# Kernel optimization log

Hardware: AMD Instinct MI355X
Metric: run time of the kernel (lower is better)

Reference implementation:

```python
import jax, jax.numpy as jnp
import numpy as np

B = 8192
IN = 1024
H = 1024


def setup_inputs() -> dict:
    key = jax.random.key(0)
    ks = jax.random.split(key, 7)
    stdv = 1.0 / np.sqrt(H)
    u = lambda k, shape: jax.random.uniform(k, shape, jnp.float32, -stdv, stdv)
    return {
        "input": jax.random.normal(ks[0], (B, IN), jnp.float32),
        "h_prev": jax.random.normal(ks[1], (B, H), jnp.float32),
        "c_prev": jax.random.normal(ks[2], (B, H), jnp.float32),
        "W_ih": u(ks[3], (4 * H, IN)),
        "b_ih": u(ks[4], (4 * H,)),
        "W_hh": u(ks[5], (4 * H, H)),
        "b_hh": u(ks[6], (4 * H,)),
    }


def reference(input, h_prev, c_prev, W_ih, b_ih, W_hh, b_hh):
    # gates: [B, 4H] = input @ W_ih^T + b_ih + h_prev @ W_hh^T + b_hh
    gates = (jnp.einsum("bi,gi->bg", input, W_ih) + b_ih
             + jnp.einsum("bh,gh->bg", h_prev, W_hh) + b_hh)
    i_in, f_in, g_in, o_in = jnp.split(gates, 4, axis=1)
    i_t = jax.nn.sigmoid(i_in)
    f_t = jax.nn.sigmoid(f_in)
    g_t = jnp.tanh(g_in)
    o_t = jax.nn.sigmoid(o_in)
    c_t = f_t * c_prev + i_t * g_t
    h_t = o_t * jnp.tanh(c_t)
    return (h_t, c_t)
```

## Files before the change

### kernel.cpp

```cpp
#include <hip/hip_runtime.h>
#include <hip/hip_bf16.h>
#include <stdint.h>


typedef __attribute__((ext_vector_type(8))) __bf16 bf16x8;
typedef __attribute__((ext_vector_type(8))) unsigned short u16x8;
typedef __attribute__((ext_vector_type(4))) float f32x4;

__device__ __forceinline__ unsigned short f2bf(float f) {
  union { float f; unsigned int u; } v; v.f = f;
  unsigned int r = v.u + 0x7FFFu + ((v.u >> 16) & 1u);
  return (unsigned short)(r >> 16);
}

__global__ void cvt_all(const float* __restrict__ s0, const float* __restrict__ s1,
                        const float* __restrict__ s2, const float* __restrict__ s3,
                        unsigned short* __restrict__ d0, unsigned short* __restrict__ d1,
                        unsigned short* __restrict__ d2, unsigned short* __restrict__ d3) {
  const float* src; unsigned short* dst; int n8;
  if (blockIdx.y == 0)      { src = s0; dst = d0; n8 = 8192 * 128; }
  else if (blockIdx.y == 1) { src = s1; dst = d1; n8 = 8192 * 128; }
  else if (blockIdx.y == 2) { src = s2; dst = d2; n8 = 4096 * 128; }
  else                      { src = s3; dst = d3; n8 = 4096 * 128; }
  int i = blockIdx.x * blockDim.x + threadIdx.x;
  int stride = gridDim.x * blockDim.x;
  for (; i < n8; i += stride) {
    float4 a = ((const float4*)src)[2 * i];
    float4 b = ((const float4*)src)[2 * i + 1];
    u16x8 o;
    o[0] = f2bf(a.x); o[1] = f2bf(a.y); o[2] = f2bf(a.z); o[3] = f2bf(a.w);
    o[4] = f2bf(b.x); o[5] = f2bf(b.y); o[6] = f2bf(b.z); o[7] = f2bf(b.w);
    *(u16x8*)&dst[(size_t)i * 8] = o;
  }
}

#define STAGE_HALF(G) do {                                                     \
    const int t_ = (G) >> 2, j_ = (G) & 3;                                     \
    const int hks_ = j_ >> 1, isB_ = j_ & 1;                                   \
    const unsigned short* bA_; const unsigned short* bB_; int kk_;             \
    if (t_ < 16) { bA_ = Xb; bB_ = Wihb; kk_ = t_ * 64; }                      \
    else         { bA_ = Hb; bB_ = Whhb; kk_ = (t_ - 16) * 64; }               \
    const int col_ = kk_ + hks_ * 32 + scol;                                   \
    char* lb_ = smem + (((G) & 7) * 16384);                                    \
    _Pragma("unroll")                                                          \
    for (int r_ = 0; r_ < 2; ++r_) {                                           \
      const int row_ = r_ * 128 + srow;                                        \
      const unsigned short* src_ = isB_                                        \
          ? bB_ + (size_t)((row_ >> 6) * 1024 + h0 + (row_ & 63)) * 1024 + col_\
          : bA_ + (size_t)(m0 + row_) * 1024 + col_;                           \
      __builtin_amdgcn_global_load_lds(                                        \
          (const __attribute__((address_space(1))) void*)src_,                 \
          (__attribute__((address_space(3))) void*)(lb_ + r_ * 8192 + tid * 16),\
          16, 0, 0);                                                           \
    }                                                                          \
  } while (0)

#define PHASE(T, B, P) do {                                                    \
    const int ks_ = (P) >> 1, mh_ = (P) & 1;                                   \
    const char* sa_ = smem + (4 * (B) + 2 * ks_) * 16384;                      \
    const char* sb_ = smem + (4 * (B) + 2 * ks_ + 1) * 16384;                  \
    bf16x8 af_[4], bf_[4];                                                     \
    _Pragma("unroll")                                                          \
    for (int m2 = 0; m2 < 4; ++m2) {                                           \
      u16x8 t8 = *(const u16x8*)(sa_ +                                         \
          ((wr * 128 + (mh_ * 4 + m2) * 16 + l15) * 64 + l4 * 16));            \
      af_[m2] = __builtin_bit_cast(bf16x8, t8);                                \
    }                                                                          \
    _Pragma("unroll")                                                          \
    for (int n_ = 0; n_ < 4; ++n_) {                                           \
      u16x8 t8 = *(const u16x8*)(sb_ +                                         \
          ((wc * 64 + n_ * 16 + l15) * 64 + l4 * 16));                         \
      bf_[n_] = __builtin_bit_cast(bf16x8, t8);                                \
    }                                                                          \
    if (4 * (T) + 6 + (P) < 128) { STAGE_HALF(4 * (T) + 6 + (P)); }            \
    __builtin_amdgcn_s_barrier();                                              \
    __builtin_amdgcn_s_setprio(1);                                             \
    _Pragma("unroll")                                                          \
    for (int m2 = 0; m2 < 4; ++m2)                                             \
      _Pragma("unroll")                                                        \
      for (int n_ = 0; n_ < 4; ++n_)                                           \
        acc[mh_ * 4 + m2][n_] = __builtin_amdgcn_mfma_f32_16x16x32_bf16(       \
            af_[m2], bf_[n_], acc[mh_ * 4 + m2][n_], 0, 0, 0);                 \
    __builtin_amdgcn_s_setprio(0);                                             \
    __builtin_amdgcn_s_barrier();                                              \
  } while (0)

#define TILE(T, B) do {                                                        \
    PHASE(T, B, 0); PHASE(T, B, 1); PHASE(T, B, 2); PHASE(T, B, 3);            \
    if ((T) < 31) {                                                            \
      if ((T) == 30) { asm volatile("s_waitcnt vmcnt(0)" ::: "memory"); }      \
      else           { asm volatile("s_waitcnt vmcnt(4)" ::: "memory"); }      \
      __builtin_amdgcn_s_barrier();                                            \
    }                                                                          \
  } while (0)

__global__ __launch_bounds__(512, 2) void lstm_fused(
    const unsigned short* __restrict__ Xb, const unsigned short* __restrict__ Hb,
    const unsigned short* __restrict__ Wihb, const unsigned short* __restrict__ Whhb,
    const float* __restrict__ bih, const float* __restrict__ bhh,
    const float* __restrict__ cprev, float* __restrict__ out) {
  __shared__ __align__(16) char smem[131072];

  const int tid = threadIdx.x;
  const int lane = tid & 63;
  const int wid = tid >> 6;
  const int wr = wid >> 2;
  const int wc = wid & 3;
  const int l15 = lane & 15;
  const int l4 = lane >> 4;

  const int bid = blockIdx.x;
  const int tile_id = (bid & 7) * 64 + (bid >> 3);
  const int m0 = (tile_id >> 4) * 256;
  const int h0 = (tile_id & 15) * 64;

  const int srow = tid >> 2;
  const int scol = (tid & 3) * 8;

  f32x4 acc[8][4];
#pragma unroll
  for (int m = 0; m < 8; ++m)
#pragma unroll
    for (int n = 0; n < 4; ++n) {
      f32x4 z = {0.f, 0.f, 0.f, 0.f};
      acc[m][n] = z;
    }

  STAGE_HALF(0); STAGE_HALF(1); STAGE_HALF(2);
  STAGE_HALF(3); STAGE_HALF(4); STAGE_HALF(5);
  asm volatile("s_waitcnt vmcnt(4)" ::: "memory");
  __builtin_amdgcn_s_barrier();

#pragma unroll 1
  for (int th = 0; th < 16; ++th) {
    const int t0 = th * 2;
    TILE(t0, 0);
    TILE(t0 + 1, 1);
  }

  __syncthreads();
#pragma unroll
  for (int ph = 0; ph < 2; ++ph) {
    if (ph) __syncthreads();
    if (wr == ph) {
#pragma unroll
      for (int m = 0; m < 8; ++m)
#pragma unroll
        for (int n = 0; n < 4; ++n)
          *(f32x4*)(smem + (((wc * 8 + m) * 4 + n) * 64 + lane) * 16) = acc[m][n];
    }
    __syncthreads();
#pragma unroll
    for (int q = 0; q < 4; ++q) {
      f32x4 vg[4];
#pragma unroll
      for (int g = 0; g < 4; ++g)
        vg[g] = *(const f32x4*)(smem + (((g * 8 + wid) * 4 + q) * 64 + lane) * 16);
      const int gcol = h0 + q * 16 + l15;
      const float b0 = bih[gcol]        + bhh[gcol];
      const float b1 = bih[1024 + gcol] + bhh[1024 + gcol];
      const float b2 = bih[2048 + gcol] + bhh[2048 + gcol];
      const float b3 = bih[3072 + gcol] + bhh[3072 + gcol];
#pragma unroll
      for (int j = 0; j < 4; ++j) {
        const size_t row = (size_t)(m0 + ph * 128 + wid * 16 + l4 * 4 + j);
        const float vi = vg[0][j] + b0;
        const float vf = vg[1][j] + b1;
        const float vgt = vg[2][j] + b2;
        const float vo = vg[3][j] + b3;
        const float si = 1.f / (1.f + __expf(-vi));
        const float sf = 1.f / (1.f + __expf(-vf));
        const float tg = tanhf(vgt);
        const float so = 1.f / (1.f + __expf(-vo));
        const float cp = cprev[row * 1024 + gcol];
        const float ct = sf * cp + si * tg;
        const float ht = so * tanhf(ct);
        out[row * 1024 + gcol] = ht;
        out[8388608 + row * 1024 + gcol] = ct;
      }
    }
  }
}

extern "C" void kernel_launch(void* const* d_in, const int* in_sizes, int n_in,
                              void* d_out, int out_size, void* d_ws, size_t ws_size,
                              hipStream_t stream) {
  const float* input  = (const float*)d_in[0];
  const float* h_prev = (const float*)d_in[1];
  const float* c_prev = (const float*)d_in[2];
  const float* W_ih   = (const float*)d_in[3];
  const float* b_ih   = (const float*)d_in[4];
  const float* W_hh   = (const float*)d_in[5];
  const float* b_hh   = (const float*)d_in[6];
  float* out = (float*)d_out;

  unsigned short* Xb   = (unsigned short*)d_ws;
  unsigned short* Hb   = Xb + (size_t)8192 * 1024;
  unsigned short* Wihb = Hb + (size_t)8192 * 1024;
  unsigned short* Whhb = Wihb + (size_t)4096 * 1024;

  dim3 cgrid(1024, 4);
  cvt_all<<<cgrid, 256, 0, stream>>>(input, h_prev, W_ih, W_hh, Xb, Hb, Wihb, Whhb);

  lstm_fused<<<512, 512, 0, stream>>>(Xb, Hb, Wihb, Whhb, b_ih, b_hh, c_prev, out);
}
```

Baseline: 353.0 us.

## Replace direct-to-LDS async loads with register-staged double buffer and XOR swizzle

Drops the global_load_lds multi-stage pipeline with per-phase barriers. Each thread now loads one 64-byte row segment into registers, writes it to a double-buffered LDS tile using an XOR swizzle to avoid bank conflicts, and syncs once per K-tile. This cuts barrier count and setprio scheduling. In exchange it uses more registers for staging, keeps less prefetch in flight, and gives less latency hiding than the prior 8-stage async scheme.

New measurement: 349.2 us. No clear change (-1.1%).

```diff
diff --git a/kernel.cpp b/kernel.cpp
--- a/kernel.cpp
+++ b/kernel.cpp
@@ -6,6 +6,7 @@
 typedef __attribute__((ext_vector_type(8))) __bf16 bf16x8;
 typedef __attribute__((ext_vector_type(8))) unsigned short u16x8;
 typedef __attribute__((ext_vector_type(4))) float f32x4;
+typedef __attribute__((ext_vector_type(4))) unsigned int u32x4;
 
 __device__ __forceinline__ unsigned short f2bf(float f) {
   union { float f; unsigned int u; } v; v.f = f;
@@ -34,64 +35,45 @@
   }
 }
 
-#define STAGE_HALF(G) do {                                                     \
-    const int t_ = (G) >> 2, j_ = (G) & 3;                                     \
-    const int hks_ = j_ >> 1, isB_ = j_ & 1;                                   \
-    const unsigned short* bA_; const unsigned short* bB_; int kk_;             \
-    if (t_ < 16) { bA_ = Xb; bB_ = Wihb; kk_ = t_ * 64; }                      \
-    else         { bA_ = Hb; bB_ = Whhb; kk_ = (t_ - 16) * 64; }               \
-    const int col_ = kk_ + hks_ * 32 + scol;                                   \
-    char* lb_ = smem + (((G) & 7) * 16384);                                    \
-    _Pragma("unroll")                                                          \
-    for (int r_ = 0; r_ < 2; ++r_) {                                           \
-      const int row_ = r_ * 128 + srow;                                        \
-      const unsigned short* src_ = isB_                                        \
-          ? bB_ + (size_t)((row_ >> 6) * 1024 + h0 + (row_ & 63)) * 1024 + col_\
-          : bA_ + (size_t)(m0 + row_) * 1024 + col_;                           \
-      __builtin_amdgcn_global_load_lds(                                        \
-          (const __attribute__((address_space(1))) void*)src_,                 \
-          (__attribute__((address_space(3))) void*)(lb_ + r_ * 8192 + tid * 16),\
-          16, 0, 0);                                                           \
-    }                                                                          \
+#define LOADHALF(T, KS) do {                                                   \
+    const unsigned short* bsrc_; int kk_;                                      \
+    if ((T) < 16) { bsrc_ = isB ? Wihb : Xb; kk_ = (T) * 64; }                 \
+    else          { bsrc_ = isB ? Whhb : Hb; kk_ = ((T) - 16) * 64; }          \
+    const unsigned short* p_ = bsrc_ + (size_t)grow_ws * 1024 + kk_ + (KS) * 32;\
+    stg[0] = *(const u32x4*)(p_);                                              \
+    stg[1] = *(const u32x4*)(p_ + 8);                                          \
+    stg[2] = *(const u32x4*)(p_ + 16);                                         \
+    stg[3] = *(const u32x4*)(p_ + 24);                                         \
   } while (0)
 
-#define PHASE(T, B, P) do {                                                    \
-    const int ks_ = (P) >> 1, mh_ = (P) & 1;                                   \
-    const char* sa_ = smem + (4 * (B) + 2 * ks_) * 16384;                      \
-    const char* sb_ = smem + (4 * (B) + 2 * ks_ + 1) * 16384;                  \
+#define DSWRITEHALF(BUF, KS) do {                                              \
+    char* wb_ = (BUF) + isB * 32768 + row_l * 128;                             \
+    *(u32x4*)(wb_ + ((((KS) * 4 + 0) ^ swz_) * 16)) = stg[0];                  \
+    *(u32x4*)(wb_ + ((((KS) * 4 + 1) ^ swz_) * 16)) = stg[1];                  \
+    *(u32x4*)(wb_ + ((((KS) * 4 + 2) ^ swz_) * 16)) = stg[2];                  \
+    *(u32x4*)(wb_ + ((((KS) * 4 + 3) ^ swz_) * 16)) = stg[3];                  \
+  } while (0)
+
+#define QUADRANT(CUR, KS, MH) do {                                             \
     bf16x8 af_[4], bf_[4];                                                     \
     _Pragma("unroll")                                                          \
     for (int m2 = 0; m2 < 4; ++m2) {                                           \
-      u16x8 t8 = *(const u16x8*)(sa_ +                                         \
-          ((wr * 128 + (mh_ * 4 + m2) * 16 + l15) * 64 + l4 * 16));            \
-      af_[m2] = __builtin_bit_cast(bf16x8, t8);                                \
+      const int ra_ = wr * 128 + ((MH) * 4 + m2) * 16 + l15;                   \
+      af_[m2] = *(const bf16x8*)((CUR) + ra_ * 128 +                           \
+                                 ((((KS) * 4 + l4) ^ (ra_ & 7)) * 16));        \
     }                                                                          \
     _Pragma("unroll")                                                          \
     for (int n_ = 0; n_ < 4; ++n_) {                                           \
-      u16x8 t8 = *(const u16x8*)(sb_ +                                         \
-          ((wc * 64 + n_ * 16 + l15) * 64 + l4 * 16));                         \
-      bf_[n_] = __builtin_bit_cast(bf16x8, t8);                                \
+      const int rb_ = wc * 64 + n_ * 16 + l15;                                 \
+      bf_[n_] = *(const bf16x8*)((CUR) + 32768 + rb_ * 128 +                   \
+                                 ((((KS) * 4 + l4) ^ (rb_ & 7)) * 16));        \
     }                                                                          \
-    if (4 * (T) + 6 + (P) < 128) { STAGE_HALF(4 * (T) + 6 + (P)); }            \
-    __builtin_amdgcn_s_barrier();                                              \
-    __builtin_amdgcn_s_setprio(1);                                             \
     _Pragma("unroll")                                                          \
     for (int m2 = 0; m2 < 4; ++m2)                                             \
       _Pragma("unroll")                                                        \
       for (int n_ = 0; n_ < 4; ++n_)                                           \
-        acc[mh_ * 4 + m2][n_] = __builtin_amdgcn_mfma_f32_16x16x32_bf16(       \
-            af_[m2], bf_[n_], acc[mh_ * 4 + m2][n_], 0, 0, 0);                 \
-    __builtin_amdgcn_s_setprio(0);                                             \
-    __builtin_amdgcn_s_barrier();                                              \
-  } while (0)
-
-#define TILE(T, B) do {                                                        \
-    PHASE(T, B, 0); PHASE(T, B, 1); PHASE(T, B, 2); PHASE(T, B, 3);            \
-    if ((T) < 31) {                                                            \
-      if ((T) == 30) { asm volatile("s_waitcnt vmcnt(0)" ::: "memory"); }      \
-      else           { asm volatile("s_waitcnt vmcnt(4)" ::: "memory"); }      \
-      __builtin_amdgcn_s_barrier();                                            \
-    }                                                                          \
+        acc[(MH) * 4 + m2][n_] = __builtin_amdgcn_mfma_f32_16x16x32_bf16(      \
+            af_[m2], bf_[n_], acc[(MH) * 4 + m2][n_], 0, 0, 0);                \
   } while (0)
 
 __global__ __launch_bounds__(512, 2) void lstm_fused(
@@ -114,8 +96,11 @@
   const int m0 = (tile_id >> 4) * 256;
   const int h0 = (tile_id & 15) * 64;
 
-  const int srow = tid >> 2;
-  const int scol = (tid & 3) * 8;
+  const int row_l = tid & 255;
+  const int isB = tid >> 8;
+  const int swz_ = row_l & 7;
+  const int grow_ws = isB ? ((row_l >> 6) * 1024 + h0 + (row_l & 63))
+                          : (m0 + row_l);
 
   f32x4 acc[8][4];
 #pragma unroll
@@ -126,16 +111,30 @@
       acc[m][n] = z;
     }
 
-  STAGE_HALF(0); STAGE_HALF(1); STAGE_HALF(2);
-  STAGE_HALF(3); STAGE_HALF(4); STAGE_HALF(5);
-  asm volatile("s_waitcnt vmcnt(4)" ::: "memory");
-  __builtin_amdgcn_s_barrier();
+  u32x4 stg[4];
+
+  LOADHALF(0, 0); DSWRITEHALF(smem, 0);
+  LOADHALF(0, 1); DSWRITEHALF(smem, 1);
+  LOADHALF(1, 0);
+  __syncthreads();
 
 #pragma unroll 1
-  for (int th = 0; th < 16; ++th) {
-    const int t0 = th * 2;
-    TILE(t0, 0);
-    TILE(t0 + 1, 1);
+  for (int t = 0; t < 32; ++t) {
+    char* cur = smem + (t & 1) * 65536;
+    char* alt = smem + ((t & 1) ^ 1) * 65536;
+    QUADRANT(cur, 0, 0);
+    QUADRANT(cur, 0, 1);
+    if (t < 31) {
+      DSWRITEHALF(alt, 0);
+      LOADHALF(t + 1, 1);
+    }
+    QUADRANT(cur, 1, 0);
+    QUADRANT(cur, 1, 1);
+    if (t < 31) {
+      DSWRITEHALF(alt, 1);
+      if (t < 30) LOADHALF(t + 2, 0);
+      __syncthreads();
+    }
   }
 
   __syncthreads();
```
